# Kernel tuning notes

Measured on AMD Instinct MI355X. Metric: run time of the kernel, lower is better.

Reference implementation:

```python
import jax, jax.numpy as jnp
import numpy as np
import math

ORDER = 4
FREQ = 160


def _layernorm(x, g, b, eps=1e-5):
    m = jnp.mean(x, axis=-1, keepdims=True)
    v = jnp.mean((x - m) ** 2, axis=-1, keepdims=True)
    return (x - m) / jnp.sqrt(v + eps) * g + b


def setup_inputs() -> dict:
    key = jax.random.key(0)
    ks = jax.random.split(key, 9)
    b, t, k, f = 8, 1000, ORDER, FREQ
    return {
        "far_complex": jax.random.normal(ks[0], (b, 2, f, t), jnp.float32),
        "mix_complex": jax.random.normal(ks[1], (b, 2, f, t), jnp.float32),
        "k_conv_w": jax.random.normal(ks[2], (2 * k, 2), jnp.float32) * 0.3,   # Conv2d(2 -> 2k, 1x1)
        "k_conv_b": jax.random.normal(ks[3], (2 * k,), jnp.float32) * 0.01,
        "ql_w": jax.random.normal(ks[4], (f, f), jnp.float32) / math.sqrt(f),  # query_linear
        "ql_b": jnp.zeros((f,), jnp.float32),
        "qn_g": jnp.ones((f,), jnp.float32),   # query_norm gamma
        "qn_b": jnp.zeros((f,), jnp.float32),  # query_norm beta
        "kl_w": jax.random.normal(ks[5], (k, k), jnp.float32) / math.sqrt(k),  # key_linear
        "kl_b": jnp.zeros((k,), jnp.float32),
        "kn_g": jnp.ones((k,), jnp.float32),
        "kn_b": jnp.zeros((k,), jnp.float32),
        "q_vec": jax.random.normal(ks[6], (f,), jnp.float32) * 0.5,  # query_vector
        "k_vec": jax.random.normal(ks[7], (k,), jnp.float32) * 0.5,  # key_vector
        "v_vec": jax.random.normal(ks[8], (k,), jnp.float32) * 0.5,  # value_vector
    }


def reference(far_complex, mix_complex, k_conv_w, k_conv_b, ql_w, ql_b,
              qn_g, qn_b, kl_w, kl_b, kn_g, kn_b, q_vec, k_vec, v_vec):
    b, c, f, t = far_complex.shape
    k = k_vec.shape[0]

    # im2col-style unfold over time with left padding (k-1)
    padded = jnp.pad(far_complex, ((0, 0), (0, 0), (0, 0), (k - 1, 0)))
    idx = jnp.arange(t)[:, None] + jnp.arange(k)[None, :]          # [t, k]
    unf = padded[..., idx]                                          # [b,2,f,t,k]
    unf_save = unf[:, 0] + 1j * unf[:, 1]                           # [b,f,t,k] complex64
    # in-place conjugation of imag channel (as in torch code)
    unf = jnp.stack([unf[:, 0], -unf[:, 1]], axis=1)                # [b,2,f,t,k]

    # per-channel outer products (torch does real matmul per channel)
    XTX = jnp.einsum('bcfti,bcftj->bcftij', unf, unf)               # [b,2,f,t,k,k]
    XTY = (unf * mix_complex[..., None])[..., None]                 # [b,2,f,t,k,1]

    query = jnp.transpose(unf, (0, 1, 3, 4, 2))                     # [b,2,t,k,f]
    kc = jnp.einsum('oc,bcft->boft', k_conv_w, mix_complex) + k_conv_b[None, :, None, None]
    key = jnp.transpose(kc.reshape(b, 2, k, f, t), (0, 1, 4, 3, 2))  # [b,2,t,f,k]

    value = jnp.swapaxes(jnp.concatenate([XTX, XTY], axis=-1), -1, -2)  # [b,2,f,t,k+1,k]

    query = _layernorm(query @ ql_w.T + ql_b, qn_g, qn_b) * jax.nn.sigmoid(q_vec)
    key = _layernorm(key @ kl_w.T + kl_b, kn_g, kn_b) * jax.nn.sigmoid(k_vec)
    value = value * jax.nn.sigmoid(v_vec)

    weight = jax.nn.softmax(query @ (key / math.sqrt(k)), axis=-1)  # [b,2,t,k,k]
    out = value @ weight[:, :, None]                                # [b,2,f,t,k+1,k]
    outT = jnp.swapaxes(out, -1, -2)                                # [b,2,f,t,k,k+1]
    XTX_new = outT[..., :k]                                         # [b,2,f,t,k,k]
    XTY_new = outT[..., k:]                                         # [b,2,f,t,k,1]
    XTX_c = XTX_new[:, 0] + 1j * XTX_new[:, 1]                      # [b,f,t,k,k]
    XTY_c = XTY_new[:, 0] + 1j * XTY_new[:, 1]                      # [b,f,t,k,1]

    eps = 1e-8
    eye_r = jnp.eye(k, dtype=jnp.float32) + eps
    eye = (eye_r + 1j * eye_r).astype(XTX_c.dtype)

    inv_XTX = jnp.linalg.inv(XTX_c + eye)                           # [b,f,t,k,k]
    wiener = (inv_XTX @ XTY_c)[..., 0]                              # [b,f,t,k]

    res = jnp.sum(unf_save * wiener, axis=-1)                       # [b,f,t]
    return jnp.stack([res.real, res.imag], axis=1)                  # [b,2,f,t]
```

## Files before the change

kernel.cpp:

```cpp
#include <hip/hip_runtime.h>
#include <math.h>

#define NBC   16
#define NF    160
#define NT    1000
#define TS    32
#define JW    48
#define QSTR  49

typedef __attribute__((ext_vector_type(8))) short short8;
typedef __attribute__((ext_vector_type(4))) float f32x4;

static __device__ __forceinline__ short f2bf(float x) {
    unsigned u = __builtin_bit_cast(unsigned, x);
    unsigned r = (u + 0x7fffu + ((u >> 16) & 1u)) >> 16;
    return (short)r;
}
static __device__ __forceinline__ float bf2f(short s) {
    unsigned u = ((unsigned)(unsigned short)s) << 16;
    return __builtin_bit_cast(float, u);
}

__global__ __launch_bounds__(640, 5) void k13_fused(const float* __restrict__ far,
                                                    const float* __restrict__ mix,
                                                    const float* __restrict__ qlw,
                                                    const float* __restrict__ qlb,
                                                    const float* __restrict__ qng,
                                                    const float* __restrict__ qnb,
                                                    const float* __restrict__ qvec,
                                                    const float* __restrict__ kcw,
                                                    const float* __restrict__ kcb,
                                                    const float* __restrict__ klw,
                                                    const float* __restrict__ klb,
                                                    const float* __restrict__ kng,
                                                    const float* __restrict__ knb,
                                                    const float* __restrict__ kvec,
                                                    float* __restrict__ W) {
    __shared__ float pool[18720];
    __shared__ float lnM[48], lnI[48];
    float* Qlds = pool;
    float* regB = pool + 7840;
    short* Bhi  = (short*)regB;
    short* Blo  = Bhi + 7680;
    float* redS = regB;
    float* redQ = regB + 1968;
    float* sbuf = regB;

    const int bc = blockIdx.x;
    const int t0 = blockIdx.y * TS;
    const int tid = threadIdx.x;
    const int w = __builtin_amdgcn_readfirstlane(tid >> 6);
    const int l = tid & 63;
    const int b = bc >> 1, c = bc & 1;
    const float sgn = c ? -1.f : 1.f;
    const float* Xb = far + (size_t)bc * NF * NT;
    const int row = l & 15;
    const int kb = l >> 4;

    short8 Ahi[5], Alo[5];
    #pragma unroll
    for (int fc = 0; fc < 5; ++fc) {
        const float* ap = qlw + (size_t)(16 * w + row) * NF + fc * 32 + kb * 8;
        float4 x0 = *(const float4*)(ap + 0);
        float4 x1 = *(const float4*)(ap + 4);
        float xv[8] = {x0.x, x0.y, x0.z, x0.w, x1.x, x1.y, x1.z, x1.w};
        short8 h, lo;
        #pragma unroll
        for (int j = 0; j < 8; ++j) {
            short hj = f2bf(xv[j]);
            h[j] = hj;
            lo[j] = f2bf(xv[j] - bf2f(hj));
        }
        Ahi[fc] = h; Alo[fc] = lo;
    }

    #pragma unroll
    for (int i = 0; i < 12; ++i) {
        int o = tid + i * 640;
        int fi = o / JW, j = o - fi * JW;
        int tq = t0 - 3 + j;
        float v = (tq >= 0 && tq < NT) ? Xb[fi * NT + tq] * sgn : 0.f;
        short hi = f2bf(v);
        short lo = f2bf(v - bf2f(hi));
        int slot = (j >> 4) * 5 + (fi >> 5);
        int sl = (((fi & 31) >> 3) << 4) | (j & 15);
        int idx = (slot * 64 + sl) * 8 + (fi & 7);
        Bhi[idx] = hi;
        Blo[idx] = lo;
    }
    __syncthreads();

    f32x4 acc0 = {0.f, 0.f, 0.f, 0.f}, acc1 = acc0, acc2 = acc0;
    #pragma unroll
    for (int fc = 0; fc < 5; ++fc) {
        #pragma unroll
        for (int tt = 0; tt < 3; ++tt) {
            short8 bh = *(const short8*)&Bhi[((tt * 5 + fc) * 64 + l) * 8];
            short8 bl = *(const short8*)&Blo[((tt * 5 + fc) * 64 + l) * 8];
            f32x4 a = (tt == 0) ? acc0 : (tt == 1) ? acc1 : acc2;
            a = __builtin_amdgcn_mfma_f32_16x16x32_bf16(Ahi[fc], bh, a, 0, 0, 0);
            a = __builtin_amdgcn_mfma_f32_16x16x32_bf16(Ahi[fc], bl, a, 0, 0, 0);
            a = __builtin_amdgcn_mfma_f32_16x16x32_bf16(Alo[fc], bh, a, 0, 0, 0);
            if (tt == 0) acc0 = a; else if (tt == 1) acc1 = a; else acc2 = a;
        }
    }
    __syncthreads();

    float qlbv[4], gam[4], bet[4];
    #pragma unroll
    for (int r = 0; r < 4; ++r) {
        int fo = 16 * w + kb * 4 + r;
        qlbv[r] = qlb[fo];
        float sq = 1.f / (1.f + expf(-qvec[fo]));
        gam[r] = qng[fo] * sq;
        bet[r] = qnb[fo] * sq;
    }
    #pragma unroll
    for (int tt = 0; tt < 3; ++tt) {
        f32x4 a = (tt == 0) ? acc0 : (tt == 1) ? acc1 : acc2;
        float v0 = a[0] + qlbv[0], v1 = a[1] + qlbv[1];
        float v2 = a[2] + qlbv[2], v3 = a[3] + qlbv[3];
        int j = tt * 16 + row;
        redS[j * 41 + w * 4 + kb] = v0 + v1 + v2 + v3;
        redQ[j * 41 + w * 4 + kb] = v0 * v0 + v1 * v1 + v2 * v2 + v3 * v3;
    }
    __syncthreads();

    if (tid < 48) {
        float s = 0.f, q = 0.f;
        #pragma unroll 8
        for (int j = 0; j < 40; ++j) {
            s += redS[tid * 41 + j];
            q += redQ[tid * 41 + j];
        }
        float mean = s * (1.f / NF);
        float var = q * (1.f / NF) - mean * mean;
        lnM[tid] = mean;
        lnI[tid] = 1.f / sqrtf(var + 1e-5f);
    }
    __syncthreads();

    #pragma unroll
    for (int tt = 0; tt < 3; ++tt) {
        f32x4 a = (tt == 0) ? acc0 : (tt == 1) ? acc1 : acc2;
        int j = tt * 16 + row;
        float mean = lnM[j], inv = lnI[j];
        #pragma unroll
        for (int r = 0; r < 4; ++r) {
            int fo = 16 * w + kb * 4 + r;
            float v = a[r] + qlbv[r];
            Qlds[fo * QSTR + j] = (v - mean) * inv * gam[r] + bet[r];
        }
    }
    __syncthreads();

    float kw0[4], kw1[4], kbv[4], klwm[16], klbv[4], kngv[4], knbv[4], sigk[4];
    #pragma unroll
    for (int j = 0; j < 4; ++j) {
        kw0[j] = kcw[(4 * c + j) * 2 + 0];
        kw1[j] = kcw[(4 * c + j) * 2 + 1];
        kbv[j] = kcb[4 * c + j];
        klbv[j] = klb[j];
        kngv[j] = kng[j];
        knbv[j] = knb[j];
        sigk[j] = 0.5f / (1.f + expf(-kvec[j]));
    }
    #pragma unroll
    for (int x = 0; x < 16; ++x) klwm[x] = klw[x];

    const int site = l & 31;
    const int h = l >> 5;
    const int t = t0 + site;
    const bool valid = t < NT;

    float s[16];
    #pragma unroll
    for (int x = 0; x < 16; ++x) s[x] = 0.f;

    const float* mix0 = mix + (size_t)(b * 2) * NF * NT;
    const float* mix1 = mix0 + (size_t)NF * NT;
    const int f0 = w * 16 + h * 8;

    if (valid) {
        #pragma unroll
        for (int ff = 0; ff < 8; ++ff) {
            int f = f0 + ff;
            float m0 = mix0[(size_t)f * NT + t];
            float m1 = mix1[(size_t)f * NT + t];
            float kraw[4], klin[4];
            #pragma unroll
            for (int j = 0; j < 4; ++j)
                kraw[j] = fmaf(kw0[j], m0, fmaf(kw1[j], m1, kbv[j]));
            #pragma unroll
            for (int jo = 0; jo < 4; ++jo) {
                float a = klbv[jo];
                #pragma unroll
                for (int ji = 0; ji < 4; ++ji) a = fmaf(klwm[jo * 4 + ji], kraw[ji], a);
                klin[jo] = a;
            }
            float mn = 0.25f * (klin[0] + klin[1] + klin[2] + klin[3]);
            float d0 = klin[0] - mn, d1 = klin[1] - mn, d2 = klin[2] - mn, d3 = klin[3] - mn;
            float var = 0.25f * (d0 * d0 + d1 * d1 + d2 * d2 + d3 * d3);
            float inv = 1.f / sqrtf(var + 1e-5f);
            float kn[4];
            kn[0] = (d0 * inv * kngv[0] + knbv[0]) * sigk[0];
            kn[1] = (d1 * inv * kngv[1] + knbv[1]) * sigk[1];
            kn[2] = (d2 * inv * kngv[2] + knbv[2]) * sigk[2];
            kn[3] = (d3 * inv * kngv[3] + knbv[3]) * sigk[3];

            float q0 = Qlds[f * QSTR + site + 0];
            float q1 = Qlds[f * QSTR + site + 1];
            float q2 = Qlds[f * QSTR + site + 2];
            float q3 = Qlds[f * QSTR + site + 3];
            #pragma unroll
            for (int j = 0; j < 4; ++j) {
                s[0 * 4 + j] = fmaf(q0, kn[j], s[0 * 4 + j]);
                s[1 * 4 + j] = fmaf(q1, kn[j], s[1 * 4 + j]);
                s[2 * 4 + j] = fmaf(q2, kn[j], s[2 * 4 + j]);
                s[3 * 4 + j] = fmaf(q3, kn[j], s[3 * 4 + j]);
            }
        }
    }

    {
        float* dst = &sbuf[((w * 2 + h) * 32 + site) * 17];
        #pragma unroll
        for (int q4 = 0; q4 < 4; ++q4) {
            float4 v = {s[q4 * 4 + 0], s[q4 * 4 + 1], s[q4 * 4 + 2], s[q4 * 4 + 3]};
            *(float4*)(dst + q4 * 4) = v;
        }
    }
    __syncthreads();

    if (tid < 128) {
        int q4 = tid >> 5;
        int ln = tid & 31;
        int tt = t0 + ln;
        if (tt < NT) {
            float4 a = *(const float4*)&sbuf[(0 * 32 + ln) * 17 + q4 * 4];
            #pragma unroll
            for (int g = 1; g < 20; ++g) {
                float4 p = *(const float4*)&sbuf[(g * 32 + ln) * 17 + q4 * 4];
                a.x += p.x; a.y += p.y; a.z += p.z; a.w += p.w;
            }
            float mx = fmaxf(fmaxf(a.x, a.y), fmaxf(a.z, a.w));
            float e0 = expf(a.x - mx), e1 = expf(a.y - mx);
            float e2 = expf(a.z - mx), e3 = expf(a.w - mx);
            float inv = 1.f / (e0 + e1 + e2 + e3);
            float4 v = {e0 * inv, e1 * inv, e2 * inv, e3 * inv};
            *(float4*)(W + ((size_t)bc * NT + tt) * 16 + q4 * 4) = v;
        }
    }
}

__device__ __forceinline__ void csolve4(float Ar[16], float Ai[16],
                                        float br[4], float bi[4],
                                        float wr[4], float wi[4]) {
    #pragma unroll
    for (int col = 0; col < 4; ++col) {
        #pragma unroll
        for (int r = col + 1; r < 4; ++r) {
            float cp = fabsf(Ar[col * 4 + col]) + fabsf(Ai[col * 4 + col]);
            float cr = fabsf(Ar[r * 4 + col]) + fabsf(Ai[r * 4 + col]);
            bool sw = cr > cp;
            #pragma unroll
            for (int m = col; m < 4; ++m) {
                float a0 = Ar[col * 4 + m], a1 = Ar[r * 4 + m];
                Ar[col * 4 + m] = sw ? a1 : a0;
                Ar[r * 4 + m]   = sw ? a0 : a1;
                float c0 = Ai[col * 4 + m], c1 = Ai[r * 4 + m];
                Ai[col * 4 + m] = sw ? c1 : c0;
                Ai[r * 4 + m]   = sw ? c0 : c1;
            }
            float b0 = br[col], b1 = br[r];
            br[col] = sw ? b1 : b0; br[r] = sw ? b0 : b1;
            float d0 = bi[col], d1 = bi[r];
            bi[col] = sw ? d1 : d0; bi[r] = sw ? d0 : d1;
        }
        float pr = Ar[col * 4 + col], pi = Ai[col * 4 + col];
        float den = 1.f / (pr * pr + pi * pi);
        #pragma unroll
        for (int r = col + 1; r < 4; ++r) {
            float nr = Ar[r * 4 + col], ni = Ai[r * 4 + col];
            float fr = (nr * pr + ni * pi) * den;
            float fi = (ni * pr - nr * pi) * den;
            #pragma unroll
            for (int m = col + 1; m < 4; ++m) {
                float tr = Ar[col * 4 + m], ti = Ai[col * 4 + m];
                Ar[r * 4 + m] -= fr * tr - fi * ti;
                Ai[r * 4 + m] -= fr * ti + fi * tr;
            }
            float tr = br[col], ti = bi[col];
            br[r] -= fr * tr - fi * ti;
            bi[r] -= fr * ti + fi * tr;
        }
    }
    #pragma unroll
    for (int col = 3; col >= 0; --col) {
        float sr = br[col], si = bi[col];
        #pragma unroll
        for (int m = col + 1; m < 4; ++m) {
            float tr = Ar[col * 4 + m], ti = Ai[col * 4 + m];
            sr -= tr * wr[m] - ti * wi[m];
            si -= tr * wi[m] + ti * wr[m];
        }
        float pr = Ar[col * 4 + col], pi = Ai[col * 4 + col];
        float den = 1.f / (pr * pr + pi * pi);
        wr[col] = (sr * pr + si * pi) * den;
        wi[col] = (si * pr - sr * pi) * den;
    }
}

__global__ __launch_bounds__(256) void k4_final(const float* __restrict__ far,
                                                const float* __restrict__ mix,
                                                const float* __restrict__ Wt,
                                                const float* __restrict__ vvec,
                                                float* __restrict__ out) {
    const int t = blockIdx.x * 256 + threadIdx.x;
    const int f = blockIdx.y;
    const int b = blockIdx.z;
    if (t >= NT) return;

    const float* fr  = far + (size_t)(b * 2 + 0) * NF * NT + (size_t)f * NT;
    const float* fim = far + (size_t)(b * 2 + 1) * NF * NT + (size_t)f * NT;
    float ur[4], ui[4];
    #pragma unroll
    for (int d = 0; d < 4; ++d) {
        int tp = t - 3 + d;
        bool ok = tp >= 0;
        ur[d] = ok ? fr[tp] : 0.f;
        ui[d] = ok ? fim[tp] : 0.f;
    }
    float m0 = mix[(size_t)(b * 2 + 0) * NF * NT + (size_t)f * NT + t];
    float m1 = mix[(size_t)(b * 2 + 1) * NF * NT + (size_t)f * NT + t];

    float sv[4];
    #pragma unroll
    for (int i = 0; i < 4; ++i) sv[i] = 1.f / (1.f + expf(-vvec[i]));

    const float* w0p = Wt + ((size_t)(b * 2 + 0) * NT + t) * 16;
    const float* w1p = Wt + ((size_t)(b * 2 + 1) * NT + t) * 16;

    float g0[4], g1[4];
    #pragma unroll
    for (int j = 0; j < 4; ++j) { g0[j] = 0.f; g1[j] = 0.f; }
    #pragma unroll
    for (int i = 0; i < 4; ++i) {
        float a0 = ur[i] * sv[i];
        float a1 = -ui[i] * sv[i];
        #pragma unroll
        for (int j = 0; j < 4; ++j) {
            g0[j] = fmaf(a0, w0p[i * 4 + j], g0[j]);
            g1[j] = fmaf(a1, w1p[i * 4 + j], g1[j]);
        }
    }

    float Ar[16], Ai[16], br[4], bi[4], wr[4], wi[4];
    #pragma unroll
    for (int j = 0; j < 4; ++j) {
        #pragma unroll
        for (int m = 0; m < 4; ++m) {
            float e = (j == m) ? (1.0f + 1e-8f) : 1e-8f;
            Ar[j * 4 + m] = fmaf(ur[m], g0[j], e);
            Ai[j * 4 + m] = fmaf(-ui[m], g1[j], e);
        }
        br[j] = m0 * g0[j];
        bi[j] = m1 * g1[j];
    }

    csolve4(Ar, Ai, br, bi, wr, wi);

    float resr = 0.f, resi = 0.f;
    #pragma unroll
    for (int d = 0; d < 4; ++d) {
        resr += ur[d] * wr[d] - ui[d] * wi[d];
        resi += ur[d] * wi[d] + ui[d] * wr[d];
    }
    out[(size_t)(b * 2 + 0) * NF * NT + (size_t)f * NT + t] = resr;
    out[(size_t)(b * 2 + 1) * NF * NT + (size_t)f * NT + t] = resi;
}

extern "C" void kernel_launch(void* const* d_in, const int* in_sizes, int n_in,
                              void* d_out, int out_size, void* d_ws, size_t ws_size,
                              hipStream_t stream) {
    const float* far  = (const float*)d_in[0];
    const float* mix  = (const float*)d_in[1];
    const float* kcw  = (const float*)d_in[2];
    const float* kcb  = (const float*)d_in[3];
    const float* qlw  = (const float*)d_in[4];
    const float* qlb  = (const float*)d_in[5];
    const float* qng  = (const float*)d_in[6];
    const float* qnb  = (const float*)d_in[7];
    const float* klw  = (const float*)d_in[8];
    const float* klb  = (const float*)d_in[9];
    const float* kng  = (const float*)d_in[10];
    const float* knb  = (const float*)d_in[11];
    const float* qvec = (const float*)d_in[12];
    const float* kvec = (const float*)d_in[13];
    const float* vvec = (const float*)d_in[14];

    float* W = (float*)d_ws;
    float* out = (float*)d_out;

    k13_fused<<<dim3(NBC, (NT + TS - 1) / TS), 640, 0, stream>>>(
        far, mix, qlw, qlb, qng, qnb, qvec, kcw, kcb, klw, klb, kng, knb, kvec, W);
    k4_final<<<dim3(4, NF, 8), 256, 0, stream>>>(far, mix, W, vvec, out);
}
```

Before: 62.14 us.

## Shrink fused query kernel to 512 threads and trim LDS footprint

Reduces the block to 8 waves, with 5 waves each computing two 16-row MFMA tiles of the query projection. The A fragments are now loaded inside the fc loop. The Q tile keeps only the 35 needed time columns and aliases all LDS regions into one smaller pool, which should allow more resident blocks. It also folds the key conv and key linear projection into a precomputed affine map per channel, so the per-frequency key work becomes 4 FMAs. The trade-offs are idle waves during the MFMA phase, an extra barrier before reusing the aliased buffer, and slightly different rounding from the folded algebra.

```diff
diff --git a/kernel.cpp b/kernel.cpp
--- a/kernel.cpp
+++ b/kernel.cpp
@@ -6,7 +6,7 @@
 #define NT    1000
 #define TS    32
 #define JW    48
-#define QSTR  49
+#define QSTR  35
 
 typedef __attribute__((ext_vector_type(8))) short short8;
 typedef __attribute__((ext_vector_type(4))) float f32x4;
@@ -21,30 +21,29 @@
     return __builtin_bit_cast(float, u);
 }
 
-__global__ __launch_bounds__(640, 5) void k13_fused(const float* __restrict__ far,
-                                                    const float* __restrict__ mix,
-                                                    const float* __restrict__ qlw,
-                                                    const float* __restrict__ qlb,
-                                                    const float* __restrict__ qng,
-                                                    const float* __restrict__ qnb,
-                                                    const float* __restrict__ qvec,
-                                                    const float* __restrict__ kcw,
-                                                    const float* __restrict__ kcb,
-                                                    const float* __restrict__ klw,
-                                                    const float* __restrict__ klb,
-                                                    const float* __restrict__ kng,
-                                                    const float* __restrict__ knb,
-                                                    const float* __restrict__ kvec,
-                                                    float* __restrict__ W) {
-    __shared__ float pool[18720];
-    __shared__ float lnM[48], lnI[48];
+__global__ __launch_bounds__(512) void k13_fused(const float* __restrict__ far,
+                                                 const float* __restrict__ mix,
+                                                 const float* __restrict__ qlw,
+                                                 const float* __restrict__ qlb,
+                                                 const float* __restrict__ qng,
+                                                 const float* __restrict__ qnb,
+                                                 const float* __restrict__ qvec,
+                                                 const float* __restrict__ kcw,
+                                                 const float* __restrict__ kcb,
+                                                 const float* __restrict__ klw,
+                                                 const float* __restrict__ klb,
+                                                 const float* __restrict__ kng,
+                                                 const float* __restrict__ knb,
+                                                 const float* __restrict__ kvec,
+                                                 float* __restrict__ W) {
+    __shared__ float pool[9600];
+    __shared__ float lnM[35], lnI[35];
+    short* Bhi  = (short*)pool;
+    short* Blo  = Bhi + 7680;
     float* Qlds = pool;
-    float* regB = pool + 7840;
-    short* Bhi  = (short*)regB;
-    short* Blo  = Bhi + 7680;
-    float* redS = regB;
-    float* redQ = regB + 1968;
-    float* sbuf = regB;
+    float* redS = pool + 5600;
+    float* redQ = pool + 5600 + 1536;
+    float* sbuf = pool;
 
     const int bc = blockIdx.x;
     const int t0 = blockIdx.y * TS;
@@ -57,29 +56,12 @@
     const int row = l & 15;
     const int kb = l >> 4;
 
-    short8 Ahi[5], Alo[5];
-    #pragma unroll
-    for (int fc = 0; fc < 5; ++fc) {
-        const float* ap = qlw + (size_t)(16 * w + row) * NF + fc * 32 + kb * 8;
-        float4 x0 = *(const float4*)(ap + 0);
-        float4 x1 = *(const float4*)(ap + 4);
-        float xv[8] = {x0.x, x0.y, x0.z, x0.w, x1.x, x1.y, x1.z, x1.w};
-        short8 h, lo;
-        #pragma unroll
-        for (int j = 0; j < 8; ++j) {
-            short hj = f2bf(xv[j]);
-            h[j] = hj;
-            lo[j] = f2bf(xv[j] - bf2f(hj));
-        }
-        Ahi[fc] = h; Alo[fc] = lo;
-    }
-
-    #pragma unroll
-    for (int i = 0; i < 12; ++i) {
-        int o = tid + i * 640;
-        int fi = o / JW, j = o - fi * JW;
+    #pragma unroll
+    for (int i = 0; i < 15; ++i) {
+        int e = tid + i * 512;
+        int fi = e / JW, j = e - fi * JW;
         int tq = t0 - 3 + j;
-        float v = (tq >= 0 && tq < NT) ? Xb[fi * NT + tq] * sgn : 0.f;
+        float v = (tq >= 0 && tq < NT) ? Xb[(size_t)fi * NT + tq] * sgn : 0.f;
         short hi = f2bf(v);
         short lo = f2bf(v - bf2f(hi));
         int slot = (j >> 4) * 5 + (fi >> 5);
@@ -90,48 +72,86 @@
     }
     __syncthreads();
 
-    f32x4 acc0 = {0.f, 0.f, 0.f, 0.f}, acc1 = acc0, acc2 = acc0;
-    #pragma unroll
-    for (int fc = 0; fc < 5; ++fc) {
+    f32x4 a00 = {0.f, 0.f, 0.f, 0.f}, a01 = a00, a02 = a00;
+    f32x4 a10 = a00, a11 = a00, a12 = a00;
+    if (w < 5) {
+        #pragma unroll
+        for (int fc = 0; fc < 5; ++fc) {
+            short8 Ah0, Al0, Ah1, Al1;
+            #pragma unroll
+            for (int g = 0; g < 2; ++g) {
+                const float* ap = qlw + (size_t)(32 * w + 16 * g + row) * NF + fc * 32 + kb * 8;
+                float4 x0 = *(const float4*)(ap + 0);
+                float4 x1 = *(const float4*)(ap + 4);
+                float xv[8] = {x0.x, x0.y, x0.z, x0.w, x1.x, x1.y, x1.z, x1.w};
+                short8 h, lo;
+                #pragma unroll
+                for (int jj = 0; jj < 8; ++jj) {
+                    short hj = f2bf(xv[jj]);
+                    h[jj] = hj;
+                    lo[jj] = f2bf(xv[jj] - bf2f(hj));
+                }
+                if (g == 0) { Ah0 = h; Al0 = lo; } else { Ah1 = h; Al1 = lo; }
+            }
+            #pragma unroll
+            for (int tt = 0; tt < 3; ++tt) {
+                short8 bh = *(const short8*)&Bhi[((tt * 5 + fc) * 64 + l) * 8];
+                short8 bl = *(const short8*)&Blo[((tt * 5 + fc) * 64 + l) * 8];
+                f32x4 a0 = (tt == 0) ? a00 : (tt == 1) ? a01 : a02;
+                a0 = __builtin_amdgcn_mfma_f32_16x16x32_bf16(Ah0, bh, a0, 0, 0, 0);
+                a0 = __builtin_amdgcn_mfma_f32_16x16x32_bf16(Ah0, bl, a0, 0, 0, 0);
+                a0 = __builtin_amdgcn_mfma_f32_16x16x32_bf16(Al0, bh, a0, 0, 0, 0);
+                if (tt == 0) a00 = a0; else if (tt == 1) a01 = a0; else a02 = a0;
+                f32x4 a1 = (tt == 0) ? a10 : (tt == 1) ? a11 : a12;
+                a1 = __builtin_amdgcn_mfma_f32_16x16x32_bf16(Ah1, bh, a1, 0, 0, 0);
+                a1 = __builtin_amdgcn_mfma_f32_16x16x32_bf16(Ah1, bl, a1, 0, 0, 0);
+                a1 = __builtin_amdgcn_mfma_f32_16x16x32_bf16(Al1, bh, a1, 0, 0, 0);
+                if (tt == 0) a10 = a1; else if (tt == 1) a11 = a1; else a12 = a1;
+            }
+        }
+    }
+    __syncthreads();
+
+    float qlbv0[4], qlbv1[4], gam0[4], gam1[4], bet0[4], bet1[4];
+    if (w < 5) {
+        #pragma unroll
+        for (int r = 0; r < 4; ++r) {
+            int fo0 = 32 * w + kb * 4 + r;
+            int fo1 = fo0 + 16;
+            qlbv0[r] = qlb[fo0];
+            qlbv1[r] = qlb[fo1];
+            float s0 = 1.f / (1.f + expf(-qvec[fo0]));
+            float s1 = 1.f / (1.f + expf(-qvec[fo1]));
+            gam0[r] = qng[fo0] * s0; bet0[r] = qnb[fo0] * s0;
+            gam1[r] = qng[fo1] * s1; bet1[r] = qnb[fo1] * s1;
+        }
         #pragma unroll
         for (int tt = 0; tt < 3; ++tt) {
-            short8 bh = *(const short8*)&Bhi[((tt * 5 + fc) * 64 + l) * 8];
-            short8 bl = *(const short8*)&Blo[((tt * 5 + fc) * 64 + l) * 8];
-            f32x4 a = (tt == 0) ? acc0 : (tt == 1) ? acc1 : acc2;
-            a = __builtin_amdgcn_mfma_f32_16x16x32_bf16(Ahi[fc], bh, a, 0, 0, 0);
-            a = __builtin_amdgcn_mfma_f32_16x16x32_bf16(Ahi[fc], bl, a, 0, 0, 0);
-            a = __builtin_amdgcn_mfma_f32_16x16x32_bf16(Alo[fc], bh, a, 0, 0, 0);
-            if (tt == 0) acc0 = a; else if (tt == 1) acc1 = a; else acc2 = a;
-        }
-    }
-    __syncthreads();
-
-    float qlbv[4], gam[4], bet[4];
-    #pragma unroll
-    for (int r = 0; r < 4; ++r) {
-        int fo = 16 * w + kb * 4 + r;
-        qlbv[r] = qlb[fo];
-        float sq = 1.f / (1.f + expf(-qvec[fo]));
-        gam[r] = qng[fo] * sq;
-        bet[r] = qnb[fo] * sq;
-    }
-    #pragma unroll
-    for (int tt = 0; tt < 3; ++tt) {
-        f32x4 a = (tt == 0) ? acc0 : (tt == 1) ? acc1 : acc2;
-        float v0 = a[0] + qlbv[0], v1 = a[1] + qlbv[1];
-        float v2 = a[2] + qlbv[2], v3 = a[3] + qlbv[3];
-        int j = tt * 16 + row;
-        redS[j * 41 + w * 4 + kb] = v0 + v1 + v2 + v3;
-        redQ[j * 41 + w * 4 + kb] = v0 * v0 + v1 * v1 + v2 * v2 + v3 * v3;
-    }
-    __syncthreads();
-
-    if (tid < 48) {
+            int j = tt * 16 + row;
+            if (j < 35) {
+                f32x4 a0 = (tt == 0) ? a00 : (tt == 1) ? a01 : a02;
+                f32x4 a1 = (tt == 0) ? a10 : (tt == 1) ? a11 : a12;
+                float v0 = a0[0] + qlbv0[0], v1 = a0[1] + qlbv0[1];
+                float v2 = a0[2] + qlbv0[2], v3 = a0[3] + qlbv0[3];
+                float u0 = a1[0] + qlbv1[0], u1 = a1[1] + qlbv1[1];
+                float u2 = a1[2] + qlbv1[2], u3 = a1[3] + qlbv1[3];
+                int s0i = j * 41 + w * 8 + kb;
+                int s1i = j * 41 + w * 8 + 4 + kb;
+                redS[s0i] = v0 + v1 + v2 + v3;
+                redQ[s0i] = v0 * v0 + v1 * v1 + v2 * v2 + v3 * v3;
+                redS[s1i] = u0 + u1 + u2 + u3;
+                redQ[s1i] = u0 * u0 + u1 * u1 + u2 * u2 + u3 * u3;
+            }
+        }
+    }
+    __syncthreads();
+
+    if (tid < 35) {
         float s = 0.f, q = 0.f;
         #pragma unroll 8
-        for (int j = 0; j < 40; ++j) {
-            s += redS[tid * 41 + j];
-            q += redQ[tid * 41 + j];
+        for (int k = 0; k < 40; ++k) {
+            s += redS[tid * 41 + k];
+            q += redQ[tid * 41 + k];
         }
         float mean = s * (1.f / NF);
         float var = q * (1.f / NF) - mean * mean;
@@ -140,36 +160,58 @@
     }
     __syncthreads();
 
-    #pragma unroll
-    for (int tt = 0; tt < 3; ++tt) {
-        f32x4 a = (tt == 0) ? acc0 : (tt == 1) ? acc1 : acc2;
-        int j = tt * 16 + row;
-        float mean = lnM[j], inv = lnI[j];
-        #pragma unroll
-        for (int r = 0; r < 4; ++r) {
-            int fo = 16 * w + kb * 4 + r;
-            float v = a[r] + qlbv[r];
-            Qlds[fo * QSTR + j] = (v - mean) * inv * gam[r] + bet[r];
-        }
-    }
-    __syncthreads();
-
-    float kw0[4], kw1[4], kbv[4], klwm[16], klbv[4], kngv[4], knbv[4], sigk[4];
-    #pragma unroll
-    for (int j = 0; j < 4; ++j) {
-        kw0[j] = kcw[(4 * c + j) * 2 + 0];
-        kw1[j] = kcw[(4 * c + j) * 2 + 1];
-        kbv[j] = kcb[4 * c + j];
-        klbv[j] = klb[j];
-        kngv[j] = kng[j];
-        knbv[j] = knb[j];
-        sigk[j] = 0.5f / (1.f + expf(-kvec[j]));
-    }
-    #pragma unroll
-    for (int x = 0; x < 16; ++x) klwm[x] = klw[x];
+    if (w < 5) {
+        #pragma unroll
+        for (int tt = 0; tt < 3; ++tt) {
+            int j = tt * 16 + row;
+            if (j < 35) {
+                f32x4 a0 = (tt == 0) ? a00 : (tt == 1) ? a01 : a02;
+                f32x4 a1 = (tt == 0) ? a10 : (tt == 1) ? a11 : a12;
+                float mean = lnM[j], inv = lnI[j];
+                #pragma unroll
+                for (int r = 0; r < 4; ++r) {
+                    int fo0 = 32 * w + kb * 4 + r;
+                    float v = a0[r] + qlbv0[r];
+                    Qlds[fo0 * QSTR + j] = (v - mean) * inv * gam0[r] + bet0[r];
+                    float u = a1[r] + qlbv1[r];
+                    Qlds[(fo0 + 16) * QSTR + j] = (u - mean) * inv * gam1[r] + bet1[r];
+                }
+            }
+        }
+    }
+    __syncthreads();
+
+    float alpha[4], beta4[4], gamm[4], G[4], H[4];
+    {
+        float M0[4], M1[4], B4[4];
+        #pragma unroll
+        for (int jo = 0; jo < 4; ++jo) {
+            float m0 = 0.f, m1 = 0.f, bb = klb[jo];
+            #pragma unroll
+            for (int ji = 0; ji < 4; ++ji) {
+                float kl = klw[jo * 4 + ji];
+                m0 = fmaf(kl, kcw[(4 * c + ji) * 2 + 0], m0);
+                m1 = fmaf(kl, kcw[(4 * c + ji) * 2 + 1], m1);
+                bb = fmaf(kl, kcb[4 * c + ji], bb);
+            }
+            M0[jo] = m0; M1[jo] = m1; B4[jo] = bb;
+        }
+        float am = 0.25f * (M0[0] + M0[1] + M0[2] + M0[3]);
+        float bm = 0.25f * (M1[0] + M1[1] + M1[2] + M1[3]);
+        float cm = 0.25f * (B4[0] + B4[1] + B4[2] + B4[3]);
+        #pragma unroll
+        for (int jo = 0; jo < 4; ++jo) {
+            alpha[jo] = M0[jo] - am;
+            beta4[jo] = M1[jo] - bm;
+            gamm[jo]  = B4[jo] - cm;
+            float sk = 0.5f / (1.f + expf(-kvec[jo]));
+            G[jo] = kng[jo] * sk;
+            H[jo] = knb[jo] * sk;
+        }
+    }
 
     const int site = l & 31;
-    const int h = l >> 5;
+    const int half = l >> 5;
     const int t = t0 + site;
     const bool valid = t < NT;
 
@@ -179,34 +221,25 @@
 
     const float* mix0 = mix + (size_t)(b * 2) * NF * NT;
     const float* mix1 = mix0 + (size_t)NF * NT;
-    const int f0 = w * 16 + h * 8;
+    const int f0 = (w * 2 + half) * 10;
 
     if (valid) {
         #pragma unroll
-        for (int ff = 0; ff < 8; ++ff) {
+        for (int ff = 0; ff < 10; ++ff) {
             int f = f0 + ff;
             float m0 = mix0[(size_t)f * NT + t];
             float m1 = mix1[(size_t)f * NT + t];
-            float kraw[4], klin[4];
-            #pragma unroll
-            for (int j = 0; j < 4; ++j)
-                kraw[j] = fmaf(kw0[j], m0, fmaf(kw1[j], m1, kbv[j]));
-            #pragma unroll
-            for (int jo = 0; jo < 4; ++jo) {
-                float a = klbv[jo];
-                #pragma unroll
-                for (int ji = 0; ji < 4; ++ji) a = fmaf(klwm[jo * 4 + ji], kraw[ji], a);
-                klin[jo] = a;
-            }
-            float mn = 0.25f * (klin[0] + klin[1] + klin[2] + klin[3]);
-            float d0 = klin[0] - mn, d1 = klin[1] - mn, d2 = klin[2] - mn, d3 = klin[3] - mn;
+            float d0 = fmaf(alpha[0], m0, fmaf(beta4[0], m1, gamm[0]));
+            float d1 = fmaf(alpha[1], m0, fmaf(beta4[1], m1, gamm[1]));
+            float d2 = fmaf(alpha[2], m0, fmaf(beta4[2], m1, gamm[2]));
+            float d3 = fmaf(alpha[3], m0, fmaf(beta4[3], m1, gamm[3]));
             float var = 0.25f * (d0 * d0 + d1 * d1 + d2 * d2 + d3 * d3);
             float inv = 1.f / sqrtf(var + 1e-5f);
             float kn[4];
-            kn[0] = (d0 * inv * kngv[0] + knbv[0]) * sigk[0];
-            kn[1] = (d1 * inv * kngv[1] + knbv[1]) * sigk[1];
-            kn[2] = (d2 * inv * kngv[2] + knbv[2]) * sigk[2];
-            kn[3] = (d3 * inv * kngv[3] + knbv[3]) * sigk[3];
+            kn[0] = fmaf(d0 * inv, G[0], H[0]);
+            kn[1] = fmaf(d1 * inv, G[1], H[1]);
+            kn[2] = fmaf(d2 * inv, G[2], H[2]);
+            kn[3] = fmaf(d3 * inv, G[3], H[3]);
 
             float q0 = Qlds[f * QSTR + site + 0];
             float q1 = Qlds[f * QSTR + site + 1];
@@ -221,9 +254,10 @@
             }
         }
     }
+    __syncthreads();
 
     {
-        float* dst = &sbuf[((w * 2 + h) * 32 + site) * 17];
+        float* dst = &sbuf[((w * 2 + half) * 32 + site) * 17];
         #pragma unroll
         for (int q4 = 0; q4 < 4; ++q4) {
             float4 v = {s[q4 * 4 + 0], s[q4 * 4 + 1], s[q4 * 4 + 2], s[q4 * 4 + 3]};
@@ -239,7 +273,7 @@
         if (tt < NT) {
             float4 a = *(const float4*)&sbuf[(0 * 32 + ln) * 17 + q4 * 4];
             #pragma unroll
-            for (int g = 1; g < 20; ++g) {
+            for (int g = 1; g < 16; ++g) {
                 float4 p = *(const float4*)&sbuf[(g * 32 + ln) * 17 + q4 * 4];
                 a.x += p.x; a.y += p.y; a.z += p.z; a.w += p.w;
             }
@@ -402,7 +436,7 @@
     float* W = (float*)d_ws;
     float* out = (float*)d_out;
 
-    k13_fused<<<dim3(NBC, (NT + TS - 1) / TS), 640, 0, stream>>>(
+    k13_fused<<<dim3(NBC, (NT + TS - 1) / TS), 512, 0, stream>>>(
         far, mix, qlw, qlb, qng, qnb, qvec, kcw, kcb, klw, klb, kng, knb, kvec, W);
     k4_final<<<dim3(4, NF, 8), 256, 0, stream>>>(far, mix, W, vvec, out);
 }
```

Measured after the change: 53.59 us. 13.8% less time.
